# Optimization experiments

Measured on AMD Instinct MI355X. Metric: run time of the kernel, lower is better.

## Reference

```python
import jax, jax.numpy as jnp
import numpy as np
from jax import lax


def _conv(x, w, b):
    # 3x3 conv, stride 1, padding 1 == SAME; NCHW / OIHW layout like torch
    y = lax.conv_general_dilated(x, w, window_strides=(1, 1), padding='SAME',
                                 dimension_numbers=('NCHW', 'OIHW', 'NCHW'))
    return y + b[None, :, None, None]


def _maxpool2(x):
    return lax.reduce_window(x, -jnp.inf, lax.max, (1, 1, 2, 2), (1, 1, 2, 2), 'VALID')


def _upsample2(x):
    # nearest-neighbor upsample, scale factor 2
    return jnp.repeat(jnp.repeat(x, 2, axis=2), 2, axis=3)


def setup_inputs() -> dict:
    key = jax.random.key(0)
    ks = jax.random.split(key, 10)
    B, H, W = 128, 128, 128
    n_codes, d = 512, 32
    s = 0.1
    return {
        'x': jax.random.normal(ks[0], (B, 1, H, W), jnp.float32),
        'w1': jax.random.normal(ks[1], (16, 1, 3, 3), jnp.float32) * s,
        'b1': jnp.zeros((16,), jnp.float32),
        'w2': jax.random.normal(ks[2], (32, 16, 3, 3), jnp.float32) * s,
        'b2': jnp.zeros((32,), jnp.float32),
        'codebook': jax.random.normal(ks[3], (n_codes, d), jnp.float32),
        'w3': jax.random.normal(ks[4], (16, 32, 3, 3), jnp.float32) * s,
        'b3': jnp.zeros((16,), jnp.float32),
        'w4': jax.random.normal(ks[5], (1, 16, 3, 3), jnp.float32) * s,
        'b4': jnp.zeros((1,), jnp.float32),
    }


def reference(x, w1, b1, w2, b2, codebook, w3, b3, w4, b4):
    # encoder
    h = jax.nn.gelu(_maxpool2(_conv(x, w1, b1)), approximate=False)
    h = _maxpool2(_conv(h, w2, b2))  # [B, 32, H/4, W/4]
    B, C, Hq, Wq = h.shape

    # VectorQuantize: euclidean nearest-code lookup on flattened fmap
    z = h.transpose(0, 2, 3, 1).reshape(B, Hq * Wq, C)  # [B, N, d]
    d2 = ((z * z).sum(-1, keepdims=True)
          - 2.0 * jnp.einsum('bnc,kc->bnk', z, codebook)
          + (codebook * codebook).sum(-1))  # [B, N, K]
    idx = jnp.argmin(d2, axis=-1)  # [B, N]
    quant = codebook[idx]  # [B, N, d]
    commit_loss = jnp.mean((lax.stop_gradient(quant) - z) ** 2)
    indices = idx.reshape(B, Hq, Wq)

    # decoder: NOTE the source discards the quantized output (x_flat) and
    # keeps feeding the pre-quantization fmap h forward; we match that.
    g = jax.nn.gelu(_conv(_upsample2(h), w3, b3), approximate=False)
    out = jnp.clip(_conv(_upsample2(g), w4, b4), -1.0, 1.0)
    return out, indices, commit_loss
```

## Files before the change

kernel.cpp:

```cpp
#include <hip/hip_runtime.h>
#include <math.h>

typedef float f32x2 __attribute__((ext_vector_type(2)));

__device__ __forceinline__ float gelu_f(float x) {
    return 0.5f * x * (1.0f + erff(x * 0.7071067811865476f));
}

__global__ __launch_bounds__(256) void kA(const float* __restrict__ x,
                                          const float* __restrict__ w1,
                                          const float* __restrict__ b1,
                                          float* __restrict__ h1,
                                          const float* __restrict__ cb,
                                          const float* __restrict__ w3,
                                          const float* __restrict__ w4,
                                          float* __restrict__ ccp,
                                          float* __restrict__ w3t,
                                          float* __restrict__ w4t,
                                          f32x2* __restrict__ w2d,
                                          const float* __restrict__ w2) {
    const int blk = blockIdx.x;
    const int t = threadIdx.x;
    if (blk >= 2048) {
        const int id = (blk - 2048) * 256 + t;
        {
            const float* row = cb + id * 32;
            float s = 0.f;
#pragma unroll
            for (int c = 0; c < 32; ++c) s += row[c] * row[c];
            ccp[id] = s;
        }
        {
            const float* w = w3 + id * 9;
            const float T00 = w[0], T01 = w[1], T02 = w[2];
            const float T10 = w[3] + w[6], T11 = w[4] + w[7], T12 = w[5] + w[8];
            const float T20 = w[0] + w[3], T21 = w[1] + w[4], T22 = w[2] + w[5];
            const float T30 = w[6], T31 = w[7], T32 = w[8];
            float* o = w3t + id * 16;
            o[0] = T00; o[1] = T00 + T01; o[2] = T01 + T02; o[3] = T02;
            o[4] = T10; o[5] = T10 + T11; o[6] = T11 + T12; o[7] = T12;
            o[8] = T20; o[9] = T20 + T21; o[10] = T21 + T22; o[11] = T22;
            o[12] = T30; o[13] = T30 + T31; o[14] = T31 + T32; o[15] = T32;
        }
        if (id < 16) {
            const float* w = w4 + id * 9;
            const float T00 = w[0], T01 = w[1], T02 = w[2];
            const float T10 = w[3] + w[6], T11 = w[4] + w[7], T12 = w[5] + w[8];
            const float T20 = w[0] + w[3], T21 = w[1] + w[4], T22 = w[2] + w[5];
            const float T30 = w[6], T31 = w[7], T32 = w[8];
            float* o = w4t + id * 16;
            o[0] = T00; o[1] = T00 + T01; o[2] = T01 + T02; o[3] = T02;
            o[4] = T10; o[5] = T10 + T11; o[6] = T11 + T12; o[7] = T12;
            o[8] = T20; o[9] = T20 + T21; o[10] = T21 + T22; o[11] = T22;
            o[12] = T30; o[13] = T30 + T31; o[14] = T31 + T32; o[15] = T32;
        }
        for (int i = id; i < 4608; i += 512) {
            const float wv = w2[i];
            w2d[i] = (f32x2){wv, wv};
        }
        return;
    }
    __shared__ float xs[34 * 38];
    const int b = blk >> 4;
    const int tile = blk & 15;
    const int ti = (tile >> 2) << 4, tj = (tile & 3) << 4;
    const float* xb = x + b * 16384;
    for (int i = t; i < 34 * 34; i += 256) {
        const int r = i / 34, c = i % 34;
        const int gr = 2 * ti - 1 + r, gc = 2 * tj - 1 + c;
        const float v = ((unsigned)gr < 128u && (unsigned)gc < 128u) ? xb[gr * 128 + gc] : 0.f;
        xs[r * 38 + (c & 1) * 19 + (c >> 1)] = v;
    }
    __syncthreads();
    const int jj = t & 15, ii = t >> 4;
    float pat[4][4];
#pragma unroll
    for (int r = 0; r < 4; r++) {
        const int row = (2 * ii + r) * 38;
        pat[r][0] = xs[row + jj];
        pat[r][1] = xs[row + 19 + jj];
        pat[r][2] = xs[row + jj + 1];
        pat[r][3] = xs[row + 20 + jj];
    }
    const int obase = b * 65536 + (ti + ii) * 64 + (tj + jj);
#pragma unroll 2
    for (int co = 0; co < 16; co++) {
        const float* wr = w1 + co * 9;
        float w[9];
#pragma unroll
        for (int k = 0; k < 9; k++) w[k] = wr[k];
        float s00 = 0.f, s01 = 0.f, s10 = 0.f, s11 = 0.f;
#pragma unroll
        for (int ty = 0; ty < 3; ty++)
#pragma unroll
            for (int tx = 0; tx < 3; tx++) {
                const float wv = w[ty * 3 + tx];
                s00 += wv * pat[ty][tx];
                s01 += wv * pat[ty][tx + 1];
                s10 += wv * pat[ty + 1][tx];
                s11 += wv * pat[ty + 1][tx + 1];
            }
        const float m = fmaxf(fmaxf(s00, s01), fmaxf(s10, s11)) + b1[co];
        h1[obase + co * 4096] = gelu_f(m);
    }
}

__global__ __launch_bounds__(256) void k_conv2(const float* __restrict__ h1,
                                               const f32x2* __restrict__ w2d,
                                               const float* __restrict__ b2,
                                               float* __restrict__ h) {
    __shared__ float hs[16 * 360];
    const int blk = blockIdx.x;
    const int b = blk >> 3;
    const int tt = blk & 7;
    const int t = threadIdx.x;
    const int co0 = __builtin_amdgcn_readfirstlane((t >> 6) << 3);
    const int lane = t & 63;
    const int irow = lane >> 3, j = lane & 7;
    const float* h1b = h1 + b * 65536;
    const f32x2* wbase = w2d + co0 * 144;
#pragma unroll 1
    for (int half = 0; half < 2; half++) {
        const int tile = tt * 2 + half;
        const int ti = (tile >> 2) << 3, tj = (tile & 3) << 3;
        if (half) __syncthreads();
        for (int i = t; i < 16 * 324; i += 256) {
            const int ci = i / 324, rc = i % 324, r = rc / 18, c = rc % 18;
            const int gr = 2 * ti - 1 + r, gc = 2 * tj - 1 + c;
            const float v = ((unsigned)gr < 64u && (unsigned)gc < 64u) ? h1b[ci * 4096 + gr * 64 + gc] : 0.f;
            hs[ci * 360 + r * 20 + (c & 1) * 10 + (c >> 1)] = v;
        }
        __syncthreads();
        f32x2 A[8], B[8];
#pragma unroll
        for (int q = 0; q < 8; q++) { A[q] = (f32x2){0.f, 0.f}; B[q] = (f32x2){0.f, 0.f}; }
#pragma unroll 4
        for (int ci = 0; ci < 16; ci++) {
            f32x2 P[4][3];
#pragma unroll
            for (int r = 0; r < 4; r++) {
                const int row = ci * 360 + (2 * irow + r) * 20;
                const float e0 = hs[row + j];
                const float o0 = hs[row + 10 + j];
                const float e1 = hs[row + j + 1];
                const float o1 = hs[row + 11 + j];
                P[r][0] = (f32x2){e0, o0};
                P[r][1] = (f32x2){o0, e1};
                P[r][2] = (f32x2){e1, o1};
            }
#pragma unroll
            for (int q = 0; q < 8; q++) {
                const f32x2* wr = wbase + q * 144 + ci * 9;
                f32x2 W[9];
#pragma unroll
                for (int k = 0; k < 9; k++) W[k] = wr[k];
#pragma unroll
                for (int ty = 0; ty < 3; ty++)
#pragma unroll
                    for (int tx = 0; tx < 3; tx++) {
                        A[q] += P[ty][tx] * W[ty * 3 + tx];
                        B[q] += P[ty + 1][tx] * W[ty * 3 + tx];
                    }
            }
        }
        float* hb = h + (b * 32 + co0) * 1024 + (ti + irow) * 32 + tj + j;
#pragma unroll
        for (int q = 0; q < 8; q++) {
            hb[q * 1024] = fmaxf(fmaxf(A[q].x, A[q].y), fmaxf(B[q].x, B[q].y)) + b2[co0 + q];
        }
    }
}

__global__ __launch_bounds__(256) void kB(const float* __restrict__ h,
                                          const float* __restrict__ w3t,
                                          const float* __restrict__ b3,
                                          float* __restrict__ g,
                                          const float* __restrict__ cb,
                                          const float* __restrict__ ccp,
                                          float* __restrict__ idx_out,
                                          float* __restrict__ pa) {
    __shared__ float smem[16 * 350];
    const int blk = blockIdx.x;
    const int t = threadIdx.x;
    if (blk < 512) {
        const int vb = blk;
        const int w = __builtin_amdgcn_readfirstlane(t >> 6);
        const int lane = t & 63;
        const int n0 = vb * 256;
        const int b = n0 >> 10;
        const int pos = (n0 & 1023) + w * 64 + lane;
        const float* hb = h + b * 32768 + pos;
        float z[32];
        float zz = 0.f;
#pragma unroll
        for (int c = 0; c < 32; ++c) {
            z[c] = hb[c * 1024];
            zz += z[c] * z[c];
        }
        f32x2 z2[16];
#pragma unroll
        for (int i = 0; i < 16; ++i) z2[i] = (f32x2){z[2 * i], z[2 * i + 1]};
        float* cbS = smem;
#pragma unroll
        for (int jj = 0; jj < 2; ++jj) {
            const float* gsrc = cb + (w * 2 + jj) * 256 + lane * 4;
            __builtin_amdgcn_global_load_lds(
                (const __attribute__((address_space(1))) void*)gsrc,
                (__attribute__((address_space(3))) void*)&cbS[(w * 2 + jj) * 256],
                16, 0, 0);
        }
        __syncthreads();
        float bd = 3.4e38f;
        int bk = 0;
        int buf = 0;
#pragma unroll 1
        for (int c = 0; c < 8; ++c) {
            if (c < 7) {
#pragma unroll
                for (int jj = 0; jj < 2; ++jj) {
                    const float* gsrc = cb + (c + 1) * 2048 + (w * 2 + jj) * 256 + lane * 4;
                    __builtin_amdgcn_global_load_lds(
                        (const __attribute__((address_space(1))) void*)gsrc,
                        (__attribute__((address_space(3))) void*)&cbS[(buf ^ 1) * 2048 + (w * 2 + jj) * 256],
                        16, 0, 0);
                }
            }
            const float* base = &cbS[buf * 2048];
#pragma unroll 4
            for (int kk2 = 0; kk2 < 32; ++kk2) {
                const int kk = c * 64 + kk2 * 2;
                const f32x2* r0 = (const f32x2*)(base + kk2 * 64);
                const f32x2* r1 = (const f32x2*)(base + kk2 * 64 + 32);
                f32x2 D0 = (f32x2){0.f, 0.f};
                f32x2 D1 = (f32x2){0.f, 0.f};
#pragma unroll
                for (int i = 0; i < 16; ++i) {
                    D0 += z2[i] * r0[i];
                    D1 += z2[i] * r1[i];
                }
                const float dot0 = D0.x + D0.y;
                const float dot1 = D1.x + D1.y;
                const float e0 = (zz - 2.f * dot0) + ccp[kk];
                const float e1 = (zz - 2.f * dot1) + ccp[kk + 1];
                if (e0 < bd) { bd = e0; bk = kk; }
                if (e1 < bd) { bd = e1; bk = kk + 1; }
            }
            __syncthreads();
            buf ^= 1;
        }
        idx_out[n0 + w * 64 + lane] = (float)bk;
        float s = bd;
#pragma unroll
        for (int m = 1; m < 64; m <<= 1) s += __shfl_xor(s, m, 64);
        if (lane == 0) pa[vb * 4 + w] = s;
        return;
    }
    float* hS = smem;
    const int cblk = blk - 512;
    const int b = cblk >> 2, strip = cblk & 3;
    const int i0 = strip * 8;
    const int co0 = __builtin_amdgcn_readfirstlane((t >> 6) << 2);
    const int lane = t & 63;
    const int rp = lane >> 3, cg = lane & 7;
    float acc[4][2][8];
#pragma unroll
    for (int cq = 0; cq < 4; cq++)
#pragma unroll
        for (int rr = 0; rr < 2; rr++)
#pragma unroll
            for (int u = 0; u < 8; u++) acc[cq][rr][u] = 0.f;
    const float* hb = h + b * 32768;
#pragma unroll 1
    for (int chunk = 0; chunk < 2; chunk++) {
        __syncthreads();
        for (int i = t; i < 16 * 340; i += 256) {
            const int cil = i / 340, rc = i % 340, r = rc / 34, c = rc % 34;
            const int gr = i0 - 1 + r, gc = c - 1;
            const float v = ((unsigned)gr < 32u && (unsigned)gc < 32u)
                ? hb[(chunk * 16 + cil) * 1024 + gr * 32 + gc] : 0.f;
            hS[cil * 350 + r * 35 + c] = v;
        }
        __syncthreads();
#pragma unroll 2
        for (int cil = 0; cil < 16; cil++) {
            const int ci = chunk * 16 + cil;
            float colr[3][6];
#pragma unroll
            for (int rr = 0; rr < 3; rr++) {
                const int rowb = cil * 350 + (rp + rr) * 35 + 4 * cg;
#pragma unroll
                for (int u = 0; u < 6; u++) colr[rr][u] = hS[rowb + u];
            }
#pragma unroll
            for (int cq = 0; cq < 4; cq++) {
                const float* wt = w3t + ((co0 + cq) * 32 + ci) * 16;
                const float T00 = wt[0], O00 = wt[1], E01 = wt[2], T02 = wt[3];
                const float T10 = wt[4], O10 = wt[5], E11 = wt[6], T12 = wt[7];
                const float T20 = wt[8], O20 = wt[9], E21 = wt[10], T22 = wt[11];
                const float T30 = wt[12], O30 = wt[13], E31 = wt[14], T32 = wt[15];
#pragma unroll
                for (int mm = 0; mm < 4; mm++) {
                    acc[cq][0][2 * mm]     += T00 * colr[0][mm] + E01 * colr[0][mm + 1] + T10 * colr[1][mm] + E11 * colr[1][mm + 1];
                    acc[cq][0][2 * mm + 1] += O00 * colr[0][mm + 1] + T02 * colr[0][mm + 2] + O10 * colr[1][mm + 1] + T12 * colr[1][mm + 2];
                    acc[cq][1][2 * mm]     += T20 * colr[1][mm] + E21 * colr[1][mm + 1] + T30 * colr[2][mm] + E31 * colr[2][mm + 1];
                    acc[cq][1][2 * mm + 1] += O20 * colr[1][mm + 1] + T22 * colr[1][mm + 2] + O30 * colr[2][mm + 1] + T32 * colr[2][mm + 2];
                }
            }
        }
    }
    const int p_e = strip * 16 + 2 * rp;
#pragma unroll
    for (int cq = 0; cq < 4; cq++) {
        const float bias = b3[co0 + cq];
        float* gb = g + (b * 16 + co0 + cq) * 4096 + p_e * 64 + 8 * cg;
#pragma unroll
        for (int rr = 0; rr < 2; rr++) {
            float4 v0, v1;
            v0.x = gelu_f(acc[cq][rr][0] + bias);
            v0.y = gelu_f(acc[cq][rr][1] + bias);
            v0.z = gelu_f(acc[cq][rr][2] + bias);
            v0.w = gelu_f(acc[cq][rr][3] + bias);
            v1.x = gelu_f(acc[cq][rr][4] + bias);
            v1.y = gelu_f(acc[cq][rr][5] + bias);
            v1.z = gelu_f(acc[cq][rr][6] + bias);
            v1.w = gelu_f(acc[cq][rr][7] + bias);
            *(float4*)(gb + rr * 64) = v0;
            *(float4*)(gb + rr * 64 + 4) = v1;
        }
    }
}

__global__ __launch_bounds__(256) void kC(const float* __restrict__ g,
                                          const float* __restrict__ w4t,
                                          const float* __restrict__ b4,
                                          float* __restrict__ out,
                                          const float* __restrict__ pa,
                                          float* __restrict__ loss) {
    __shared__ float smem[8 * 690];
    const int blk = blockIdx.x;
    const int t = threadIdx.x;
    if (blk >= 1024) {
        float s = 0.f;
        for (int i = t; i < 2048; i += 256) s += pa[i];
        smem[t] = s;
        __syncthreads();
        for (int off = 128; off > 0; off >>= 1) {
            if (t < off) smem[t] += smem[t + off];
            __syncthreads();
        }
        if (t == 0) loss[0] = smem[0] * (1.0f / 4194304.0f);
        return;
    }
    float* gS = smem;
    const int b = blk >> 3, strip = blk & 7;
    const int i0 = strip * 8;
    const int rp = t >> 5, cg = t & 31;
    float acc[2][4];
#pragma unroll
    for (int rr = 0; rr < 2; rr++)
#pragma unroll
        for (int u = 0; u < 4; u++) acc[rr][u] = 0.f;
    const float* gbs = g + b * 65536;
#pragma unroll 1
    for (int chunk = 0; chunk < 2; chunk++) {
        __syncthreads();
        for (int i = t; i < 8 * 660; i += 256) {
            const int cil = i / 660, rc = i % 660, r = rc / 66, c = rc % 66;
            const int gr = i0 - 1 + r, gc = c - 1;
            const float v = ((unsigned)gr < 64u && (unsigned)gc < 64u)
                ? gbs[(chunk * 8 + cil) * 4096 + gr * 64 + gc] : 0.f;
            gS[cil * 690 + r * 69 + c] = v;
        }
        __syncthreads();
#pragma unroll 2
        for (int cil = 0; cil < 8; cil++) {
            const int ci = chunk * 8 + cil;
            float colv[3][4];
#pragma unroll
            for (int rr = 0; rr < 3; rr++) {
                const int rowb = cil * 690 + (rp + rr) * 69 + 2 * cg;
#pragma unroll
                for (int u = 0; u < 4; u++) colv[rr][u] = gS[rowb + u];
            }
            const float* wt = w4t + ci * 16;
            const float T00 = wt[0], O00 = wt[1], E01 = wt[2], T02 = wt[3];
            const float T10 = wt[4], O10 = wt[5], E11 = wt[6], T12 = wt[7];
            const float T20 = wt[8], O20 = wt[9], E21 = wt[10], T22 = wt[11];
            const float T30 = wt[12], O30 = wt[13], E31 = wt[14], T32 = wt[15];
#pragma unroll
            for (int mm = 0; mm < 2; mm++) {
                acc[0][2 * mm]     += T00 * colv[0][mm] + E01 * colv[0][mm + 1] + T10 * colv[1][mm] + E11 * colv[1][mm + 1];
                acc[0][2 * mm + 1] += O00 * colv[0][mm + 1] + T02 * colv[0][mm + 2] + O10 * colv[1][mm + 1] + T12 * colv[1][mm + 2];
                acc[1][2 * mm]     += T20 * colv[1][mm] + E21 * colv[1][mm + 1] + T30 * colv[2][mm] + E31 * colv[2][mm + 1];
                acc[1][2 * mm + 1] += O20 * colv[1][mm + 1] + T22 * colv[1][mm + 2] + O30 * colv[2][mm + 1] + T32 * colv[2][mm + 2];
            }
        }
    }
    const float bias = b4[0];
    const int p_e = strip * 16 + 2 * rp;
    float* ob = out + b * 16384 + p_e * 128 + 4 * cg;
#pragma unroll
    for (int rr = 0; rr < 2; rr++) {
        float4 v;
        v.x = fminf(fmaxf(acc[rr][0] + bias, -1.f), 1.f);
        v.y = fminf(fmaxf(acc[rr][1] + bias, -1.f), 1.f);
        v.z = fminf(fmaxf(acc[rr][2] + bias, -1.f), 1.f);
        v.w = fminf(fmaxf(acc[rr][3] + bias, -1.f), 1.f);
        *(float4*)(ob + rr * 128) = v;
    }
}

extern "C" void kernel_launch(void* const* d_in, const int* in_sizes, int n_in,
                              void* d_out, int out_size, void* d_ws, size_t ws_size,
                              hipStream_t stream) {
    const float* x  = (const float*)d_in[0];
    const float* w1 = (const float*)d_in[1];
    const float* b1 = (const float*)d_in[2];
    const float* w2 = (const float*)d_in[3];
    const float* b2 = (const float*)d_in[4];
    const float* cb = (const float*)d_in[5];
    const float* w3 = (const float*)d_in[6];
    const float* b3 = (const float*)d_in[7];
    const float* w4 = (const float*)d_in[8];
    const float* b4 = (const float*)d_in[9];

    float* ws = (float*)d_ws;
    float* h1 = ws;
    float* h  = ws + 8388608;
    float* g  = h1;
    float* ccp = ws + 12582912;
    float* pa  = ws + 12583424;
    float* w4t = ws + 12585472;

    float* outp = (float*)d_out;
    float* w3t = outp;
    f32x2* w2d = (f32x2*)(outp + 8192);
    float* idx = outp + 2097152;
    float* loss = outp + 2228224;

    kA<<<2050, 256, 0, stream>>>(x, w1, b1, h1, cb, w3, w4, ccp, w3t, w4t, w2d, w2);
    k_conv2<<<1024, 256, 0, stream>>>(h1, w2d, b2, h);
    kB<<<1024, 256, 0, stream>>>(h, w3t, b3, g, cb, ccp, idx, pa);
    kC<<<1025, 256, 0, stream>>>(g, w4t, b4, outp, pa, loss);
}
```

Before: 219.6 us.

## Split VQ codebook search across four blocks with packed 64-bit atomicMin reduction

The nearest-code search now splits the 512-entry codebook into four 128-entry slices, each handled by its own block, so there are four times as many VQ blocks and each loads its slice into LDS in one go with no double buffering. Per-slice minima are packed as an order-preserving float key plus index into a 64-bit atomicMin on a workspace array, which kA initialises. The final kernel's loss block decodes the keys, writes the indices and sums the distances. This raises parallelism and removes the serial pipelined chunk loop. In exchange it adds atomics, a 1 MB key-array initialise and read, and a serial 512-iteration loop in a single reduction block.

```diff
diff --git a/kernel.cpp b/kernel.cpp
--- a/kernel.cpp
+++ b/kernel.cpp
@@ -18,7 +18,8 @@
                                           float* __restrict__ w3t,
                                           float* __restrict__ w4t,
                                           f32x2* __restrict__ w2d,
-                                          const float* __restrict__ w2) {
+                                          const float* __restrict__ w2,
+                                          unsigned long long* __restrict__ minkey) {
     const int blk = blockIdx.x;
     const int t = threadIdx.x;
     if (blk >= 2048) {
@@ -58,6 +59,7 @@
             const float wv = w2[i];
             w2d[i] = (f32x2){wv, wv};
         }
+        for (int i = id; i < 131072; i += 512) minkey[i] = 0xFFFFFFFFFFFFFFFFull;
         return;
     }
     __shared__ float xs[34 * 38];
@@ -177,18 +179,16 @@
                                           float* __restrict__ g,
                                           const float* __restrict__ cb,
                                           const float* __restrict__ ccp,
-                                          float* __restrict__ idx_out,
-                                          float* __restrict__ pa) {
+                                          unsigned long long* __restrict__ minkey) {
     __shared__ float smem[16 * 350];
     const int blk = blockIdx.x;
     const int t = threadIdx.x;
-    if (blk < 512) {
-        const int vb = blk;
+    if (blk < 2048) {
+        const int nchunk = blk >> 2, ks = blk & 3;
         const int w = __builtin_amdgcn_readfirstlane(t >> 6);
         const int lane = t & 63;
-        const int n0 = vb * 256;
-        const int b = n0 >> 10;
-        const int pos = (n0 & 1023) + w * 64 + lane;
+        const int n = nchunk * 256 + t;
+        const int b = n >> 10, pos = n & 1023;
         const float* hb = h + b * 32768 + pos;
         float z[32];
         float zz = 0.f;
@@ -197,66 +197,54 @@
             z[c] = hb[c * 1024];
             zz += z[c] * z[c];
         }
-        f32x2 z2[16];
-#pragma unroll
-        for (int i = 0; i < 16; ++i) z2[i] = (f32x2){z[2 * i], z[2 * i + 1]};
         float* cbS = smem;
-#pragma unroll
-        for (int jj = 0; jj < 2; ++jj) {
-            const float* gsrc = cb + (w * 2 + jj) * 256 + lane * 4;
+        const float* cbb = cb + (ks << 12);
+#pragma unroll
+        for (int jj = 0; jj < 4; ++jj) {
+            const float* gsrc = cbb + (w * 4 + jj) * 256 + lane * 4;
             __builtin_amdgcn_global_load_lds(
                 (const __attribute__((address_space(1))) void*)gsrc,
-                (__attribute__((address_space(3))) void*)&cbS[(w * 2 + jj) * 256],
+                (__attribute__((address_space(3))) void*)&cbS[(w * 4 + jj) * 256],
                 16, 0, 0);
         }
         __syncthreads();
+        const float* ccb = ccp + (ks << 7);
+        const int kbase = ks << 7;
         float bd = 3.4e38f;
         int bk = 0;
-        int buf = 0;
 #pragma unroll 1
-        for (int c = 0; c < 8; ++c) {
-            if (c < 7) {
-#pragma unroll
-                for (int jj = 0; jj < 2; ++jj) {
-                    const float* gsrc = cb + (c + 1) * 2048 + (w * 2 + jj) * 256 + lane * 4;
-                    __builtin_amdgcn_global_load_lds(
-                        (const __attribute__((address_space(1))) void*)gsrc,
-                        (__attribute__((address_space(3))) void*)&cbS[(buf ^ 1) * 2048 + (w * 2 + jj) * 256],
-                        16, 0, 0);
-                }
-            }
-            const float* base = &cbS[buf * 2048];
-#pragma unroll 4
-            for (int kk2 = 0; kk2 < 32; ++kk2) {
-                const int kk = c * 64 + kk2 * 2;
-                const f32x2* r0 = (const f32x2*)(base + kk2 * 64);
-                const f32x2* r1 = (const f32x2*)(base + kk2 * 64 + 32);
-                f32x2 D0 = (f32x2){0.f, 0.f};
-                f32x2 D1 = (f32x2){0.f, 0.f};
-#pragma unroll
-                for (int i = 0; i < 16; ++i) {
-                    D0 += z2[i] * r0[i];
-                    D1 += z2[i] * r1[i];
-                }
-                const float dot0 = D0.x + D0.y;
-                const float dot1 = D1.x + D1.y;
-                const float e0 = (zz - 2.f * dot0) + ccp[kk];
-                const float e1 = (zz - 2.f * dot1) + ccp[kk + 1];
-                if (e0 < bd) { bd = e0; bk = kk; }
-                if (e1 < bd) { bd = e1; bk = kk + 1; }
-            }
-            __syncthreads();
-            buf ^= 1;
-        }
-        idx_out[n0 + w * 64 + lane] = (float)bk;
-        float s = bd;
-#pragma unroll
-        for (int m = 1; m < 64; m <<= 1) s += __shfl_xor(s, m, 64);
-        if (lane == 0) pa[vb * 4 + w] = s;
+        for (int kk = 0; kk < 128; kk += 2) {
+            const float4* R0 = (const float4*)(cbS + (kk << 5));
+            const float4* R1 = (const float4*)(cbS + (kk << 5) + 32);
+            float d0a = 0.f, d0b = 0.f, d1a = 0.f, d1b = 0.f;
+#pragma unroll
+            for (int jq = 0; jq < 8; ++jq) {
+                const float4 q0 = R0[jq];
+                const float4 q1 = R1[jq];
+                d0a += z[4 * jq] * q0.x;
+                d0b += z[4 * jq + 1] * q0.y;
+                d0a += z[4 * jq + 2] * q0.z;
+                d0b += z[4 * jq + 3] * q0.w;
+                d1a += z[4 * jq] * q1.x;
+                d1b += z[4 * jq + 1] * q1.y;
+                d1a += z[4 * jq + 2] * q1.z;
+                d1b += z[4 * jq + 3] * q1.w;
+            }
+            const float dot0 = d0a + d0b;
+            const float dot1 = d1a + d1b;
+            const float e0 = (zz - 2.f * dot0) + ccb[kk];
+            const float e1 = (zz - 2.f * dot1) + ccb[kk + 1];
+            if (e0 < bd) { bd = e0; bk = kbase + kk; }
+            if (e1 < bd) { bd = e1; bk = kbase + kk + 1; }
+        }
+        const unsigned u = __float_as_uint(bd);
+        const unsigned m = (u & 0x80000000u) ? ~u : (u | 0x80000000u);
+        const unsigned long long key = (((unsigned long long)m) << 32) | (unsigned)bk;
+        atomicMin(&minkey[n], key);
         return;
     }
     float* hS = smem;
-    const int cblk = blk - 512;
+    const int cblk = blk - 2048;
     const int b = cblk >> 2, strip = cblk & 3;
     const int i0 = strip * 8;
     const int co0 = __builtin_amdgcn_readfirstlane((t >> 6) << 2);
@@ -334,14 +322,23 @@
                                           const float* __restrict__ w4t,
                                           const float* __restrict__ b4,
                                           float* __restrict__ out,
-                                          const float* __restrict__ pa,
+                                          const unsigned long long* __restrict__ minkey,
+                                          float* __restrict__ idx_out,
                                           float* __restrict__ loss) {
     __shared__ float smem[8 * 690];
     const int blk = blockIdx.x;
     const int t = threadIdx.x;
     if (blk >= 1024) {
         float s = 0.f;
-        for (int i = t; i < 2048; i += 256) s += pa[i];
+#pragma unroll 1
+        for (int i = 0; i < 512; ++i) {
+            const int n = i * 256 + t;
+            const unsigned long long key = minkey[n];
+            idx_out[n] = (float)(unsigned)(key & 0xFFFFFFFFu);
+            const unsigned m = (unsigned)(key >> 32);
+            const unsigned u = (m & 0x80000000u) ? (m ^ 0x80000000u) : ~m;
+            s += __uint_as_float(u);
+        }
         smem[t] = s;
         __syncthreads();
         for (int off = 128; off > 0; off >>= 1) {
@@ -429,8 +426,8 @@
     float* h  = ws + 8388608;
     float* g  = h1;
     float* ccp = ws + 12582912;
-    float* pa  = ws + 12583424;
-    float* w4t = ws + 12585472;
+    float* w4t = ws + 12583424;
+    unsigned long long* minkey = (unsigned long long*)(ws + 12583680);
 
     float* outp = (float*)d_out;
     float* w3t = outp;
@@ -438,8 +435,8 @@
     float* idx = outp + 2097152;
     float* loss = outp + 2228224;
 
-    kA<<<2050, 256, 0, stream>>>(x, w1, b1, h1, cb, w3, w4, ccp, w3t, w4t, w2d, w2);
+    kA<<<2050, 256, 0, stream>>>(x, w1, b1, h1, cb, w3, w4, ccp, w3t, w4t, w2d, w2, minkey);
     k_conv2<<<1024, 256, 0, stream>>>(h1, w2d, b2, h);
-    kB<<<1024, 256, 0, stream>>>(h, w3t, b3, g, cb, ccp, idx, pa);
-    kC<<<1025, 256, 0, stream>>>(g, w4t, b4, outp, pa, loss);
-}
+    kB<<<2560, 256, 0, stream>>>(h, w3t, b3, g, cb, ccp, minkey);
+    kC<<<1025, 256, 0, stream>>>(g, w4t, b4, outp, minkey, idx, loss);
+}
```

Measured after the change: 348.0 us. 1.58x slower.

## Split VQ from conv3 and hold codebook in registers with wave-level argmin

Applied to the files above, without the earlier changes.

Separates the fused VQ/conv3 kernel into two launches. The VQ kernel now stages z vectors in LDS and gives each lane 4 codebook rows in registers per pass. For each position it computes distances and takes the argmin across the wave with shuffles. This replaces per-thread sequential scans over codebook rows streamed through LDS. It adds 6 shuffle rounds per position and an extra kernel launch, and gives up the overlap between VQ and conv3 work inside one grid.

```diff
diff --git a/kernel.cpp b/kernel.cpp
--- a/kernel.cpp
+++ b/kernel.cpp
@@ -171,92 +171,98 @@
     }
 }
 
-__global__ __launch_bounds__(256) void kB(const float* __restrict__ h,
-                                          const float* __restrict__ w3t,
-                                          const float* __restrict__ b3,
-                                          float* __restrict__ g,
-                                          const float* __restrict__ cb,
-                                          const float* __restrict__ ccp,
-                                          float* __restrict__ idx_out,
-                                          float* __restrict__ pa) {
-    __shared__ float smem[16 * 350];
+__global__ __launch_bounds__(256, 2) void k_vq(const float* __restrict__ h,
+                                               const float* __restrict__ cb,
+                                               const float* __restrict__ ccp,
+                                               float* __restrict__ idx_out,
+                                               float* __restrict__ pa) {
+    __shared__ float zT[256 * 32];
+    __shared__ float zzS[256];
     const int blk = blockIdx.x;
     const int t = threadIdx.x;
-    if (blk < 512) {
-        const int vb = blk;
-        const int w = __builtin_amdgcn_readfirstlane(t >> 6);
-        const int lane = t & 63;
-        const int n0 = vb * 256;
-        const int b = n0 >> 10;
-        const int pos = (n0 & 1023) + w * 64 + lane;
+    const int w = __builtin_amdgcn_readfirstlane(t >> 6);
+    const int lane = t & 63;
+    const int n0 = blk * 256;
+    const int b = blk >> 2;
+    const int pos = (blk & 3) * 256 + t;
+    {
         const float* hb = h + b * 32768 + pos;
         float z[32];
         float zz = 0.f;
 #pragma unroll
-        for (int c = 0; c < 32; ++c) {
-            z[c] = hb[c * 1024];
-            zz += z[c] * z[c];
-        }
-        f32x2 z2[16];
-#pragma unroll
-        for (int i = 0; i < 16; ++i) z2[i] = (f32x2){z[2 * i], z[2 * i + 1]};
-        float* cbS = smem;
-#pragma unroll
-        for (int jj = 0; jj < 2; ++jj) {
-            const float* gsrc = cb + (w * 2 + jj) * 256 + lane * 4;
-            __builtin_amdgcn_global_load_lds(
-                (const __attribute__((address_space(1))) void*)gsrc,
-                (__attribute__((address_space(3))) void*)&cbS[(w * 2 + jj) * 256],
-                16, 0, 0);
-        }
-        __syncthreads();
-        float bd = 3.4e38f;
-        int bk = 0;
-        int buf = 0;
+        for (int c = 0; c < 32; ++c) { z[c] = hb[c * 1024]; zz += z[c] * z[c]; }
+#pragma unroll
+        for (int q = 0; q < 8; ++q) {
+            *(float4*)&zT[t * 32 + 4 * q] = make_float4(z[4 * q], z[4 * q + 1], z[4 * q + 2], z[4 * q + 3]);
+        }
+        zzS[t] = zz;
+    }
+    float st_d = 3.4e38f;
+    int st_k = 0;
 #pragma unroll 1
-        for (int c = 0; c < 8; ++c) {
-            if (c < 7) {
-#pragma unroll
-                for (int jj = 0; jj < 2; ++jj) {
-                    const float* gsrc = cb + (c + 1) * 2048 + (w * 2 + jj) * 256 + lane * 4;
-                    __builtin_amdgcn_global_load_lds(
-                        (const __attribute__((address_space(1))) void*)gsrc,
-                        (__attribute__((address_space(3))) void*)&cbS[(buf ^ 1) * 2048 + (w * 2 + jj) * 256],
-                        16, 0, 0);
+    for (int pass = 0; pass < 2; ++pass) {
+        float4 cbr[4][8];
+        float cc[4];
+#pragma unroll
+        for (int j = 0; j < 4; ++j) {
+            const float* ck = cb + (pass * 256 + j * 64 + lane) * 32;
+#pragma unroll
+            for (int q = 0; q < 8; ++q) cbr[j][q] = *(const float4*)(ck + 4 * q);
+            cc[j] = ccp[pass * 256 + j * 64 + lane];
+        }
+#pragma unroll 1
+        for (int i = 0; i < 64; ++i) {
+            const int row = w * 64 + i;
+            const float* zr = &zT[row * 32];
+            float4 zv[8];
+#pragma unroll
+            for (int q = 0; q < 8; ++q) zv[q] = *(const float4*)(zr + 4 * q);
+            const float zz = zzS[row];
+            float e[4];
+#pragma unroll
+            for (int j = 0; j < 4; ++j) {
+                float d0a = 0.f, d0b = 0.f;
+#pragma unroll
+                for (int q = 0; q < 8; ++q) {
+                    d0a += zv[q].x * cbr[j][q].x;
+                    d0b += zv[q].y * cbr[j][q].y;
+                    d0a += zv[q].z * cbr[j][q].z;
+                    d0b += zv[q].w * cbr[j][q].w;
                 }
-            }
-            const float* base = &cbS[buf * 2048];
-#pragma unroll 4
-            for (int kk2 = 0; kk2 < 32; ++kk2) {
-                const int kk = c * 64 + kk2 * 2;
-                const f32x2* r0 = (const f32x2*)(base + kk2 * 64);
-                const f32x2* r1 = (const f32x2*)(base + kk2 * 64 + 32);
-                f32x2 D0 = (f32x2){0.f, 0.f};
-                f32x2 D1 = (f32x2){0.f, 0.f};
-#pragma unroll
-                for (int i = 0; i < 16; ++i) {
-                    D0 += z2[i] * r0[i];
-                    D1 += z2[i] * r1[i];
-                }
-                const float dot0 = D0.x + D0.y;
-                const float dot1 = D1.x + D1.y;
-                const float e0 = (zz - 2.f * dot0) + ccp[kk];
-                const float e1 = (zz - 2.f * dot1) + ccp[kk + 1];
-                if (e0 < bd) { bd = e0; bk = kk; }
-                if (e1 < bd) { bd = e1; bk = kk + 1; }
-            }
-            __syncthreads();
-            buf ^= 1;
-        }
-        idx_out[n0 + w * 64 + lane] = (float)bk;
-        float s = bd;
-#pragma unroll
-        for (int m = 1; m < 64; m <<= 1) s += __shfl_xor(s, m, 64);
-        if (lane == 0) pa[vb * 4 + w] = s;
-        return;
-    }
-    float* hS = smem;
-    const int cblk = blk - 512;
+                e[j] = (zz - 2.f * (d0a + d0b)) + cc[j];
+            }
+            float bd = e[0];
+            int bk = pass * 256 + lane;
+#pragma unroll
+            for (int j = 1; j < 4; ++j) {
+                const int kj = pass * 256 + j * 64 + lane;
+                if (e[j] < bd) { bd = e[j]; bk = kj; }
+            }
+#pragma unroll
+            for (int m = 1; m < 64; m <<= 1) {
+                const float od = __shfl_xor(bd, m, 64);
+                const int ok = __shfl_xor(bk, m, 64);
+                if (od < bd || (od == bd && ok < bk)) { bd = od; bk = ok; }
+            }
+            if (lane == i) {
+                if (bd < st_d) { st_d = bd; st_k = bk; }
+            }
+        }
+    }
+    idx_out[n0 + w * 64 + lane] = (float)st_k;
+    float s = st_d;
+#pragma unroll
+    for (int m = 1; m < 64; m <<= 1) s += __shfl_xor(s, m, 64);
+    if (lane == 0) pa[blk * 4 + w] = s;
+}
+
+__global__ __launch_bounds__(256) void k_conv3(const float* __restrict__ h,
+                                               const float* __restrict__ w3t,
+                                               const float* __restrict__ b3,
+                                               float* __restrict__ g) {
+    __shared__ float hS[16 * 350];
+    const int cblk = blockIdx.x;
+    const int t = threadIdx.x;
     const int b = cblk >> 2, strip = cblk & 3;
     const int i0 = strip * 8;
     const int co0 = __builtin_amdgcn_readfirstlane((t >> 6) << 2);
@@ -440,6 +446,7 @@
 
     kA<<<2050, 256, 0, stream>>>(x, w1, b1, h1, cb, w3, w4, ccp, w3t, w4t, w2d, w2);
     k_conv2<<<1024, 256, 0, stream>>>(h1, w2d, b2, h);
-    kB<<<1024, 256, 0, stream>>>(h, w3t, b3, g, cb, ccp, idx, pa);
+    k_vq<<<512, 256, 0, stream>>>(h, cb, ccp, idx, pa);
+    k_conv3<<<512, 256, 0, stream>>>(h, w3t, b3, g);
     kC<<<1025, 256, 0, stream>>>(g, w4t, b4, outp, pa, loss);
 }
```

Result: slower. 304.5 us (+38.7%).
